# Kernel optimization log

Hardware: AMD Instinct MI355X
Metric: run time of the kernel (lower is better)

Reference implementation:

```python
import jax, jax.numpy as jnp
import numpy as np

IMAGE_SIZE = 800
OUT = 50          # feature map size
FEAT = 512
SCALES = (2.0, 4.0, 6.0)
RATIOS = (0.5, 1.0, 1.5)
A = len(SCALES) * len(RATIOS)          # 9 anchors per cell
POS_THR, NEG_THR = 0.7, 0.3
W_CONF, W_REG = 1.0, 5.0
SCALE = IMAGE_SIZE // OUT              # 16, stride of feature map


def _anchor_base():
    # order: ratio outer loop, scale inner loop (matches get_anchor_base)
    ws = jnp.array([s * r for r in RATIOS for s in SCALES], jnp.float32)  # [A]
    hs = jnp.array([s for r in RATIOS for s in SCALES], jnp.float32)      # [A]
    cx = (jnp.arange(OUT, dtype=jnp.float32) + 0.5)[:, None, None]        # grid dim0 -> x
    cy = (jnp.arange(OUT, dtype=jnp.float32) + 0.5)[None, :, None]        # grid dim1 -> y
    xmin = jnp.clip(cx - ws / 2, 0.0, OUT)
    xmax = jnp.clip(cx + ws / 2, 0.0, OUT)
    ymin = jnp.clip(cy - hs / 2, 0.0, OUT)
    ymax = jnp.clip(cy + hs / 2, 0.0, OUT)
    shp = (OUT, OUT, A)
    base = jnp.stack([jnp.broadcast_to(xmin, shp), jnp.broadcast_to(ymin, shp),
                      jnp.broadcast_to(xmax, shp), jnp.broadcast_to(ymax, shp)], axis=-1)
    return base.reshape(-1, 4)         # [N,4], N = OUT*OUT*A = 22500


def _iou(anchors, gt):
    # anchors [N,4], gt [B,M,4] (xyxy) -> iou [B,N,M]
    a = anchors[None, :, None, :]
    g = gt[:, None, :, :]
    ix1 = jnp.maximum(a[..., 0], g[..., 0]); iy1 = jnp.maximum(a[..., 1], g[..., 1])
    ix2 = jnp.minimum(a[..., 2], g[..., 2]); iy2 = jnp.minimum(a[..., 3], g[..., 3])
    inter = jnp.clip(ix2 - ix1, 0.0) * jnp.clip(iy2 - iy1, 0.0)
    area_a = (a[..., 2] - a[..., 0]) * (a[..., 3] - a[..., 1])
    area_g = (g[..., 2] - g[..., 0]) * (g[..., 3] - g[..., 1])
    return inter / (area_a + area_g - inter + 1e-8)


def _smooth_l1(d):
    ad = jnp.abs(d)
    return jnp.where(ad < 1.0, 0.5 * d * d, ad - 0.5)


def setup_inputs() -> dict:
    key = jax.random.key(0)
    ks = jax.random.split(key, 8)
    B, M = 16, 16
    features = jax.random.normal(ks[0], (B, FEAT, OUT, OUT), jnp.float32)
    # valid GT boxes in image coords: centers in [100,700], sizes in [32,200]
    cxy = jax.random.uniform(ks[1], (B, M, 2), jnp.float32, 100.0, 700.0)
    wh = jax.random.uniform(ks[2], (B, M, 2), jnp.float32, 32.0, 200.0)
    x1y1 = jnp.clip(cxy - wh / 2, 0.0, IMAGE_SIZE)
    x2y2 = jnp.clip(cxy + wh / 2, 0.0, IMAGE_SIZE)
    gt_boxes = jnp.concatenate([x1y1, x2y2], axis=-1)
    w1 = jax.random.normal(ks[3], (FEAT, FEAT, 3, 3), jnp.float32) * 0.02
    b1 = jnp.zeros((FEAT,), jnp.float32)
    w_cls = jax.random.normal(ks[4], (A, FEAT), jnp.float32) * 0.02
    b_cls = jnp.zeros((A,), jnp.float32)
    w_box = jax.random.normal(ks[5], (4 * A, FEAT), jnp.float32) * 0.02
    b_box = jnp.zeros((4 * A,), jnp.float32)
    return {"features": features, "gt_boxes": gt_boxes, "w1": w1, "b1": b1,
            "w_cls": w_cls, "b_cls": b_cls, "w_box": w_box, "b_box": b_box}


def reference(features, gt_boxes, w1, b1, w_cls, b_cls, w_box, b_box):
    B = features.shape[0]
    anchors = _anchor_base()                                   # [N,4]
    N = anchors.shape[0]

    # --- conv tower ---
    x = jax.lax.conv_general_dilated(features, w1, (1, 1), 'SAME') + b1[None, :, None, None]
    cls_map = jnp.einsum('bchw,ac->bahw', x, w_cls) + b_cls[None, :, None, None]   # [B,A,H,W]
    box_map = jnp.einsum('bchw,dc->bdhw', x, w_box) + b_box[None, :, None, None]   # [B,4A,H,W]
    logits = jnp.transpose(cls_map, (0, 2, 3, 1)).reshape(B, N)                    # [B,N]
    pred_off = jnp.transpose(box_map.reshape(B, A, 4, OUT, OUT), (0, 3, 4, 1, 2)).reshape(B, N, 4)

    # --- project gt to feature-map (anchor) coords, 'p2a' ---
    gt = gt_boxes / SCALE                                       # [B,M,4]

    # --- anchor/GT assignment ---
    iou = _iou(anchors, gt)                                     # [B,N,M]
    max_per_gt = jnp.max(iou, axis=1, keepdims=True)            # best anchor per gt
    pos_mask = ((iou == max_per_gt) & (max_per_gt > 0)) | (iou > POS_THR)  # [B,N,M]
    pos_mask = pos_mask.astype(jnp.float32)
    n_pos = jnp.maximum(pos_mask.sum(), 1.0)

    # --- gt offsets (standard tx,ty,tw,th) for every (anchor,gt) pair ---
    acx = (anchors[:, 0] + anchors[:, 2]) / 2
    acy = (anchors[:, 1] + anchors[:, 3]) / 2
    aw = jnp.maximum(anchors[:, 2] - anchors[:, 0], 1e-6)
    ah = jnp.maximum(anchors[:, 3] - anchors[:, 1], 1e-6)
    gcx = (gt[..., 0] + gt[..., 2]) / 2                         # [B,M]
    gcy = (gt[..., 1] + gt[..., 3]) / 2
    gw = jnp.maximum(gt[..., 2] - gt[..., 0], 1e-6)
    gh = jnp.maximum(gt[..., 3] - gt[..., 1], 1e-6)
    tx = (gcx[:, None, :] - acx[None, :, None]) / aw[None, :, None]   # [B,N,M]
    ty = (gcy[:, None, :] - acy[None, :, None]) / ah[None, :, None]
    tw = jnp.log(gw[:, None, :] / aw[None, :, None])
    th = jnp.log(gh[:, None, :] / ah[None, :, None])
    gt_off = jnp.stack([tx, ty, tw, th], axis=-1)               # [B,N,M,4]

    diff = gt_off - pred_off[:, :, None, :]
    reg_loss = (pos_mask[..., None] * _smooth_l1(diff)).sum() / (4.0 * n_pos)

    # --- classification loss: BCE-with-logits; positives=1, negatives=0 ---
    pos_loss = (pos_mask * jax.nn.softplus(-logits)[:, :, None]).sum() / n_pos
    neg_anchor = jnp.all(iou < NEG_THR, axis=2).astype(jnp.float32)   # [B,N]
    n_neg = jnp.maximum(neg_anchor.sum(), 1.0)
    neg_loss = (neg_anchor * jax.nn.softplus(logits)).sum() / n_neg
    cls_loss = 0.5 * (pos_loss + neg_loss)

    total_rpn_loss = W_CONF * cls_loss + W_REG * reg_loss

    # --- proposals from predicted offsets for all anchors ---
    pcx = acx[None, :] + pred_off[..., 0] * aw[None, :]
    pcy = acy[None, :] + pred_off[..., 1] * ah[None, :]
    pw = aw[None, :] * jnp.exp(pred_off[..., 2])
    ph = ah[None, :] * jnp.exp(pred_off[..., 3])
    proposals = jnp.stack([pcx - pw / 2, pcy - ph / 2, pcx + pw / 2, pcy + ph / 2], axis=-1)  # [B,N,4]

    return total_rpn_loss, proposals
```

## Files before the change

kernel.cpp:

```cpp
#include <hip/hip_runtime.h>
#include <hip/hip_bf16.h>
#include <stdint.h>

using bf16x8 = __attribute__((ext_vector_type(8))) __bf16;
using f32x4  = __attribute__((ext_vector_type(4))) float;

#define FT_POS_B 1024
#define W2_CHUNK_B 34560

__device__ __forceinline__ unsigned short f2bf(float f) {
  union { float f; unsigned u; } x; x.f = f;
  unsigned r = x.u + 0x7fffu + ((x.u >> 16) & 1u);
  return (unsigned short)(r >> 16);
}

__device__ __forceinline__ void gl_lds16(const void* g, void* l) {
  __builtin_amdgcn_global_load_lds(
      (const __attribute__((address_space(1))) void*)g,
      (__attribute__((address_space(3))) void*)l, 16, 0, 0);
}

__device__ __forceinline__ float sl1(float d) {
  float ad = fabsf(d);
  return ad < 1.f ? 0.5f * d * d : ad - 0.5f;
}
__device__ __forceinline__ float softplus_f(float x) {
  return fmaxf(x, 0.f) + log1pf(expf(-fabsf(x)));
}

__device__ __forceinline__ void anchor_strict(int n, float& ax1, float& ay1,
                                              float& ax2, float& ay2) {
  int ii = n / 450;
  int rem = n - ii * 450;
  int jj = rem / 9;
  int a  = rem - jj * 9;
  const float SC[3] = {2.f, 4.f, 6.f};
  const float RA[3] = {0.5f, 1.f, 1.5f};
  float w = __fmul_rn(SC[a % 3], RA[a / 3]);
  float h = SC[a % 3];
  float cx = __fadd_rn((float)ii, 0.5f);
  float cy = __fadd_rn((float)jj, 0.5f);
  float wh = __fmul_rn(w, 0.5f), hh = __fmul_rn(h, 0.5f);
  ax1 = fminf(fmaxf(__fsub_rn(cx, wh), 0.f), 50.f);
  ax2 = fminf(fmaxf(__fadd_rn(cx, wh), 0.f), 50.f);
  ay1 = fminf(fmaxf(__fsub_rn(cy, hh), 0.f), 50.f);
  ay2 = fminf(fmaxf(__fadd_rn(cy, hh), 0.f), 50.f);
}
__device__ __forceinline__ float iou_strict(float ax1, float ay1, float ax2, float ay2,
                                            float aarea, const float* __restrict__ g) {
  float gx1 = __fmul_rn(g[0], 0.0625f), gy1 = __fmul_rn(g[1], 0.0625f);
  float gx2 = __fmul_rn(g[2], 0.0625f), gy2 = __fmul_rn(g[3], 0.0625f);
  float ix1 = fmaxf(ax1, gx1), iy1 = fmaxf(ay1, gy1);
  float ix2 = fminf(ax2, gx2), iy2 = fminf(ay2, gy2);
  float inter = __fmul_rn(fmaxf(__fsub_rn(ix2, ix1), 0.f),
                          fmaxf(__fsub_rn(iy2, iy1), 0.f));
  float garea = __fmul_rn(__fsub_rn(gx2, gx1), __fsub_rn(gy2, gy1));
  float denom = __fadd_rn(__fsub_rn(__fadd_rn(aarea, garea), inter), 1e-8f);
  return __fdiv_rn(inter, denom);
}

__global__ __launch_bounds__(256) void k_featT(const float* __restrict__ feat,
                                               char* __restrict__ featT2) {
  const int tile = blockIdx.x;
  const int h    = blockIdx.y;
  const int b    = blockIdx.z;
  const int tid  = threadIdx.x;
  if (tile == 79) {
    uint4 z = {0, 0, 0, 0};
    for (int u = tid; u < 204 * 8; u += 256) {
      int p = u >> 3, rec = u & 7;
      int ip, jp;
      if (p < 52)       { ip = 0;       jp = p; }
      else if (p < 104) { ip = 51;      jp = p - 52; }
      else if (p < 154) { ip = p - 103; jp = 0; }
      else              { ip = p - 153; jp = 51; }
      char* dst = featT2 + (size_t)((b * 52 + ip) * 52 + jp) * FT_POS_B
                + (h * 8 + rec) * 64;
      *(uint4*)(dst)      = z;
      *(uint4*)(dst + 16) = z;
      *(uint4*)(dst + 32) = z;
      *(uint4*)(dst + 48) = z;
    }
    return;
  }
  __shared__ __align__(16) unsigned short sT[32][264];
  const int pos0 = tile * 32;
  const float* fb = feat + (size_t)b * 1280000 + (size_t)h * 256 * 2500;
  const int psub = (tid & 7) * 4;
  const int cio  = tid >> 3;
#pragma unroll
  for (int it = 0; it < 8; ++it) {
    int ci = it * 32 + cio;
    int p = pos0 + psub;
    float4 v;
    if (p + 3 < 2500) {
      v = *(const float4*)(fb + (size_t)ci * 2500 + p);
    } else {
      v.x = fb[(size_t)ci * 2500 + min(p + 0, 2499)];
      v.y = fb[(size_t)ci * 2500 + min(p + 1, 2499)];
      v.z = fb[(size_t)ci * 2500 + min(p + 2, 2499)];
      v.w = fb[(size_t)ci * 2500 + min(p + 3, 2499)];
    }
    sT[psub + 0][ci] = f2bf(v.x);
    sT[psub + 1][ci] = f2bf(v.y);
    sT[psub + 2][ci] = f2bf(v.z);
    sT[psub + 3][ci] = f2bf(v.w);
  }
  __syncthreads();
  {
    int p = tid >> 3, rec = tid & 7;
    int gp = pos0 + p;
    if (gp < 2500) {
      int i = gp / 50, j = gp - i * 50;
      char* dst = featT2 + (size_t)((b * 52 + i + 1) * 52 + (j + 1)) * FT_POS_B
                + (h * 8 + rec) * 64;
      const uint4* src = (const uint4*)&sT[p][rec * 32];
      uint4 a0 = src[0], a1 = src[1], a2 = src[2], a3 = src[3];
      *(uint4*)(dst)      = a0;
      *(uint4*)(dst + 16) = a1;
      *(uint4*)(dst + 32) = a2;
      *(uint4*)(dst + 48) = a3;
    }
  }
}

__global__ __launch_bounds__(128) void k_weff1(const float* __restrict__ w1,
                                               const float* __restrict__ wc,
                                               const float* __restrict__ wb,
                                               float* __restrict__ part) {
  __shared__ float sW[48][64];
  const int t = threadIdx.x;
  const int kmem = blockIdx.x * 128 + t;
  const int cz = blockIdx.y;
#pragma unroll
  for (int q = 0; q < 24; ++q) {
    int idx = t + q * 128;
    int co = idx >> 6, cl = idx & 63;
    int c = cz * 64 + cl;
    float v = 0.f;
    if (co < 9) v = wc[co * 512 + c];
    else if (co < 45) v = wb[(co - 9) * 512 + c];
    sW[co][cl] = v;
  }
  __syncthreads();
  float acc[48];
#pragma unroll
  for (int co = 0; co < 48; ++co) acc[co] = 0.f;
  const float* w1p = w1 + (size_t)(cz * 64) * 4608 + kmem;
  for (int c4 = 0; c4 < 64; c4 += 4) {
    float f0 = w1p[(size_t)(c4 + 0) * 4608];
    float f1 = w1p[(size_t)(c4 + 1) * 4608];
    float f2 = w1p[(size_t)(c4 + 2) * 4608];
    float f3 = w1p[(size_t)(c4 + 3) * 4608];
#pragma unroll
    for (int co = 0; co < 48; ++co) {
      float4 wv = *(const float4*)&sW[co][c4];
      acc[co] += wv.x * f0 + wv.y * f1 + wv.z * f2 + wv.w * f3;
    }
  }
  float* dst = part + (size_t)cz * 221184 + kmem;
#pragma unroll
  for (int co = 0; co < 48; ++co) dst[(size_t)co * 4608] = acc[co];
}

__global__ __launch_bounds__(256) void k_weff2(const float* __restrict__ part,
                                               unsigned short* __restrict__ w2) {
  int idx = blockIdx.x * 256 + threadIdx.x;
  int c = idx / 17280;  int r = idx - c * 17280;
  int tap = r / 1920;   int r2 = r - tap * 1920;
  int co = r2 / 40;     int e = r2 - co * 40;
  float s = 0.f;
  if (e < 32) {
    int ci = c * 32 + e;
    const float* p = part + (size_t)co * 4608 + ci * 9 + tap;
#pragma unroll
    for (int cz = 0; cz < 8; ++cz) s += p[(size_t)cz * 221184];
  }
  w2[idx] = f2bf(s);
}

__global__ __launch_bounds__(64) void k_bias(const float* __restrict__ wc,
                                             const float* __restrict__ wb,
                                             const float* __restrict__ b1,
                                             const float* __restrict__ bc,
                                             const float* __restrict__ bbx,
                                             float* __restrict__ bias_eff) {
  int co = blockIdx.x, l = threadIdx.x;
  float s = 0.f;
#pragma unroll
  for (int q = 0; q < 8; ++q) {
    int c = q * 64 + l;
    float wv = co < 9 ? wc[co * 512 + c] : (co < 45 ? wb[(co - 9) * 512 + c] : 0.f);
    s += wv * b1[c];
  }
  for (int o = 32; o; o >>= 1) s += __shfl_down(s, o, 64);
  if (l == 0)
    bias_eff[co] = s + (co < 9 ? bc[co] : (co < 45 ? bbx[co - 9] : 0.f));
}

__global__ __launch_bounds__(256) void k_iou(const float* __restrict__ gt_boxes,
                                             unsigned* __restrict__ mx) {
  int b = blockIdx.y;
  int n = blockIdx.x * 256 + threadIdx.x;
  float lm[16];
#pragma unroll
  for (int m = 0; m < 16; ++m) lm[m] = 0.f;
  if (n < 22500) {
    float ax1, ay1, ax2, ay2;
    anchor_strict(n, ax1, ay1, ax2, ay2);
    float aarea = __fmul_rn(__fsub_rn(ax2, ax1), __fsub_rn(ay2, ay1));
#pragma unroll
    for (int m = 0; m < 16; ++m)
      lm[m] = iou_strict(ax1, ay1, ax2, ay2, aarea, gt_boxes + (b * 16 + m) * 4);
  }
  __shared__ float red[4][16];
#pragma unroll
  for (int m = 0; m < 16; ++m) {
    float v = lm[m];
    for (int o = 32; o; o >>= 1) v = fmaxf(v, __shfl_down(v, o, 64));
    if ((threadIdx.x & 63) == 0) red[threadIdx.x >> 6][m] = v;
  }
  __syncthreads();
  if (threadIdx.x < 16) {
    float v = fmaxf(fmaxf(red[0][threadIdx.x], red[1][threadIdx.x]),
                    fmaxf(red[2][threadIdx.x], red[3][threadIdx.x]));
    atomicMax(mx + b * 16 + threadIdx.x, __float_as_uint(v));
  }
}

__global__ __launch_bounds__(256) void k_conv(const char* __restrict__ featT2,
                                              const char* __restrict__ w2,
                                              const float* __restrict__ beff,
                                              float* __restrict__ oh) {
  __shared__ __align__(16) char sF[2][19456];
  __shared__ __align__(16) char sA[2][34816];
  const int tid = threadIdx.x, lane = tid & 63, w = tid >> 6;
  const int bx = blockIdx.x;
  const int b = bx >> 4, tl = bx & 15, tr = tl >> 2, tc = tl & 3;
  const int i0 = tr * 13 - (tr == 3 ? 1 : 0);
  const int TI = (tr >= 2) ? 12 : 13;
  const int j0 = tc * 13 - (tc == 3 ? 1 : 0);
  const int TJ = (tc >= 2) ? 12 : 13;
  const int TJ2 = TJ + 2;
  const int mcount = TI * TJ;
  const int pieces = (TI + 2) * TJ2 * 5;

  const char* srcF[5];
#pragma unroll
  for (int k = 0; k < 5; ++k) {
    int s = w * 5 + k;
    int pi = s * 64 + lane;
    if (pi >= pieces) pi = pieces - 1;
    int pos = pi / 5, pc = pi - pos * 5;
    if (pc > 3) pc = 3;
    int hi = pos / TJ2, hj = pos - hi * TJ2;
    srcF[k] = featT2 + (size_t)((b * 52 + i0 + hi) * 52 + (j0 + hj)) * FT_POS_B + pc * 16;
  }
  int idxB[3];
#pragma unroll
  for (int bf = 0; bf < 3; ++bf) {
    int p = (w * 3 + bf) * 16 + (lane & 15);
    if (p >= mcount) p = mcount - 1;
    int di = p / TJ, dj = p - di * TJ;
    idxB[bf] = (di * TJ2 + dj) * 80 + (lane >> 4) * 16;
  }
  const int aoff = (lane & 15) * 80 + (lane >> 4) * 16;
  int toff[9];
#pragma unroll
  for (int tp = 0; tp < 9; ++tp) toff[tp] = ((tp / 3) * TJ2 + (tp % 3)) * 80;

  f32x4 acc[3][3] = {};

  auto stage = [&](int c, int pb) {
#pragma unroll
    for (int k = 0; k < 5; ++k) {
      int s = w * 5 + k;
      if (s < 18) gl_lds16(srcF[k] + (size_t)c * 64, sF[pb] + s * 1024);
    }
#pragma unroll
    for (int k = 0; k < 9; ++k) {
      int s = w + 4 * k;
      if (s < 34)
        gl_lds16(w2 + (size_t)c * W2_CHUNK_B + s * 1024 + lane * 16, sA[pb] + s * 1024);
    }
  };

  stage(0, 0);
  __builtin_amdgcn_s_waitcnt(0);
  __syncthreads();

  for (int c = 0; c < 16; ++c) {
    int pb = c & 1;
    if (c < 15) stage(c + 1, pb ^ 1);
    const char* fA = sA[pb];
    const char* fB = sF[pb];
#pragma unroll
    for (int tp = 0; tp < 9; ++tp) {
      bf16x8 av[3], bv[3];
#pragma unroll
      for (int cf = 0; cf < 3; ++cf)
        av[cf] = *(const bf16x8*)(fA + tp * 3840 + cf * 1280 + aoff);
#pragma unroll
      for (int bf = 0; bf < 3; ++bf)
        bv[bf] = *(const bf16x8*)(fB + idxB[bf] + toff[tp]);
#pragma unroll
      for (int cf = 0; cf < 3; ++cf)
#pragma unroll
        for (int bf = 0; bf < 3; ++bf)
          acc[cf][bf] = __builtin_amdgcn_mfma_f32_16x16x32_bf16(av[cf], bv[bf], acc[cf][bf], 0, 0, 0);
    }
    __builtin_amdgcn_s_waitcnt(0);
    __syncthreads();
  }

  f32x4 bias[3];
#pragma unroll
  for (int cf = 0; cf < 3; ++cf)
    bias[cf] = *(const f32x4*)(beff + cf * 16 + (lane >> 4) * 4);
#pragma unroll
  for (int bf = 0; bf < 3; ++bf) {
    int p = (w * 3 + bf) * 16 + (lane & 15);
    if (p >= mcount) continue;
    int di = p / TJ, dj = p - di * TJ;
    int gm = (b * 50 + i0 + di) * 50 + (j0 + dj);
#pragma unroll
    for (int cf = 0; cf < 3; ++cf) {
      f32x4 v = acc[cf][bf];
#pragma unroll
      for (int r = 0; r < 4; ++r) v[r] += bias[cf][r];
      *(f32x4*)(oh + (size_t)gm * 48 + cf * 16 + (lane >> 4) * 4) = v;
    }
  }
}

__global__ __launch_bounds__(256) void k_loss(const float* __restrict__ gt_boxes,
                                              const unsigned* __restrict__ mxbuf,
                                              const float* __restrict__ oh,
                                              float* __restrict__ accum,
                                              float* __restrict__ dout) {
  int b = blockIdx.y;
  int n = blockIdx.x * 256 + threadIdx.x;
  float s_np = 0.f, s_reg = 0.f, s_pos = 0.f, s_nc = 0.f, s_nl = 0.f;
  if (n < 22500) {
    float ax1, ay1, ax2, ay2;
    anchor_strict(n, ax1, ay1, ax2, ay2);
    float aarea = __fmul_rn(__fsub_rn(ax2, ax1), __fsub_rn(ay2, ay1));
    float acx = (ax1 + ax2) * 0.5f, acy = (ay1 + ay2) * 0.5f;
    float aw = fmaxf(ax2 - ax1, 1e-6f), ah = fmaxf(ay2 - ay1, 1e-6f);
    int ii = n / 450, rem = n - ii * 450, jj = rem / 9, a = rem - jj * 9;
    const float* row = oh + ((size_t)(b * 2500 + ii * 50 + jj)) * 48;
    float logit = row[a];
    float p0 = row[9 + a * 4], p1 = row[10 + a * 4];
    float p2 = row[11 + a * 4], p3 = row[12 + a * 4];
    int npos = 0;
    bool allneg = true;
#pragma unroll
    for (int m = 0; m < 16; ++m) {
      const float* g = gt_boxes + (b * 16 + m) * 4;
      float iou = iou_strict(ax1, ay1, ax2, ay2, aarea, g);
      float mxv = __uint_as_float(mxbuf[b * 16 + m]);
      bool pos = ((iou == mxv) && (mxv > 0.f)) || (iou > 0.7f);
      if (iou >= 0.3f) allneg = false;
      if (pos) {
        ++npos;
        float gx1 = g[0] * 0.0625f, gy1 = g[1] * 0.0625f;
        float gx2 = g[2] * 0.0625f, gy2 = g[3] * 0.0625f;
        float gcx = (gx1 + gx2) * 0.5f, gcy = (gy1 + gy2) * 0.5f;
        float gw = fmaxf(gx2 - gx1, 1e-6f), gh = fmaxf(gy2 - gy1, 1e-6f);
        float tx = (gcx - acx) / aw, ty = (gcy - acy) / ah;
        float twv = logf(gw / aw), thv = logf(gh / ah);
        s_reg += sl1(tx - p0) + sl1(ty - p1) + sl1(twv - p2) + sl1(thv - p3);
      }
    }
    s_np = (float)npos;
    s_pos = (float)npos * softplus_f(-logit);
    if (allneg) { s_nc = 1.f; s_nl = softplus_f(logit); }
    float pcx = acx + p0 * aw, pcy = acy + p1 * ah;
    float pw = aw * expf(p2), ph = ah * expf(p3);
    float* o = dout + 1 + ((size_t)b * 22500 + n) * 4;
    o[0] = pcx - pw * 0.5f;
    o[1] = pcy - ph * 0.5f;
    o[2] = pcx + pw * 0.5f;
    o[3] = pcy + ph * 0.5f;
  }
  float vals[5] = {s_np, s_reg, s_pos, s_nc, s_nl};
  __shared__ float red[4][5];
#pragma unroll
  for (int q = 0; q < 5; ++q) {
    float v = vals[q];
    for (int o = 32; o; o >>= 1) v += __shfl_down(v, o, 64);
    if ((threadIdx.x & 63) == 0) red[threadIdx.x >> 6][q] = v;
  }
  __syncthreads();
  if (threadIdx.x < 5) {
    float v = red[0][threadIdx.x] + red[1][threadIdx.x] +
              red[2][threadIdx.x] + red[3][threadIdx.x];
    atomicAdd(accum + threadIdx.x, v);
  }
}

__global__ void k_fin(const float* __restrict__ accum, float* __restrict__ dout) {
  if (threadIdx.x == 0 && blockIdx.x == 0) {
    float np = fmaxf(accum[0], 1.f);
    float nn = fmaxf(accum[3], 1.f);
    float loss = 0.5f * (accum[2] / np + accum[4] / nn) + 5.f * (accum[1] / (4.f * np));
    dout[0] = loss;
  }
}

extern "C" void kernel_launch(void* const* d_in, const int* in_sizes, int n_in,
                              void* d_out, int out_size, void* d_ws, size_t ws_size,
                              hipStream_t stream) {
  const float* features = (const float*)d_in[0];
  const float* gt_boxes = (const float*)d_in[1];
  const float* w1    = (const float*)d_in[2];
  const float* b1    = (const float*)d_in[3];
  const float* w_cls = (const float*)d_in[4];
  const float* b_cls = (const float*)d_in[5];
  const float* w_box = (const float*)d_in[6];
  const float* b_box = (const float*)d_in[7];
  float* out = (float*)d_out;
  char* ws = (char*)d_ws;

  char*           featT2 = ws;
  unsigned short* w2     = (unsigned short*)(ws + 44302336);
  float*          wpart  = (float*)(ws + 44855296);
  float*          oh     = (float*)(ws + 51933184);
  float*          beff   = (float*)(ws + 59613184);
  unsigned*       mx     = (unsigned*)(ws + 59613376);
  float*          accum  = (float*)(ws + 59614400);

  hipMemsetAsync(ws + 59613376, 0, 1056, stream);

  k_featT<<<dim3(80, 2, 16), 256, 0, stream>>>(features, featT2);
  k_weff1<<<dim3(36, 8), 128, 0, stream>>>(w1, w_cls, w_box, wpart);
  k_weff2<<<1080, 256, 0, stream>>>(wpart, w2);
  k_bias<<<48, 64, 0, stream>>>(w_cls, w_box, b1, b_cls, b_box, beff);
  k_iou<<<dim3(88, 16), 256, 0, stream>>>(gt_boxes, mx);
  k_conv<<<256, 256, 0, stream>>>(featT2, (const char*)w2, beff, oh);
  k_loss<<<dim3(88, 16), 256, 0, stream>>>(gt_boxes, mx, oh, accum, out);
  k_fin<<<1, 64, 0, stream>>>(accum, out);
}
```

Baseline: 276.1 us.

## Retile feature transpose and fold memset and bias kernel into others

The feature transpose now uses 128-position by 128-channel tiles with packed ushort4 LDS writes instead of 32-position by 256-channel tiles, which cuts the block count and widens the shared-memory stores. The separate hipMemsetAsync is replaced by zeroing inside the first k_weff1 block, and the k_bias kernel is merged into extra blocks of k_weff2. Together these remove two launches and the memset from the stream. The risk is that the zeroing now depends on k_weff1 running before k_iou, which stream order guarantees, and the LDS row stride of 132 may cause bank conflicts.

```diff
diff --git a/kernel.cpp b/kernel.cpp
--- a/kernel.cpp
+++ b/kernel.cpp
@@ -62,20 +62,20 @@
 __global__ __launch_bounds__(256) void k_featT(const float* __restrict__ feat,
                                                char* __restrict__ featT2) {
   const int tile = blockIdx.x;
-  const int h    = blockIdx.y;
+  const int g    = blockIdx.y;
   const int b    = blockIdx.z;
   const int tid  = threadIdx.x;
-  if (tile == 79) {
+  if (tile == 20) {
     uint4 z = {0, 0, 0, 0};
-    for (int u = tid; u < 204 * 8; u += 256) {
-      int p = u >> 3, rec = u & 7;
+    for (int u = tid; u < 204 * 4; u += 256) {
+      int p = u >> 2, c4 = u & 3;
       int ip, jp;
       if (p < 52)       { ip = 0;       jp = p; }
       else if (p < 104) { ip = 51;      jp = p - 52; }
       else if (p < 154) { ip = p - 103; jp = 0; }
       else              { ip = p - 153; jp = 51; }
       char* dst = featT2 + (size_t)((b * 52 + ip) * 52 + jp) * FT_POS_B
-                + (h * 8 + rec) * 64;
+                + (g * 4 + c4) * 64;
       *(uint4*)(dst)      = z;
       *(uint4*)(dst + 16) = z;
       *(uint4*)(dst + 32) = z;
@@ -83,53 +83,65 @@
     }
     return;
   }
-  __shared__ __align__(16) unsigned short sT[32][264];
-  const int pos0 = tile * 32;
-  const float* fb = feat + (size_t)b * 1280000 + (size_t)h * 256 * 2500;
-  const int psub = (tid & 7) * 4;
-  const int cio  = tid >> 3;
-#pragma unroll
-  for (int it = 0; it < 8; ++it) {
-    int ci = it * 32 + cio;
-    int p = pos0 + psub;
-    float4 v;
-    if (p + 3 < 2500) {
-      v = *(const float4*)(fb + (size_t)ci * 2500 + p);
-    } else {
-      v.x = fb[(size_t)ci * 2500 + min(p + 0, 2499)];
-      v.y = fb[(size_t)ci * 2500 + min(p + 1, 2499)];
-      v.z = fb[(size_t)ci * 2500 + min(p + 2, 2499)];
-      v.w = fb[(size_t)ci * 2500 + min(p + 3, 2499)];
-    }
-    sT[psub + 0][ci] = f2bf(v.x);
-    sT[psub + 1][ci] = f2bf(v.y);
-    sT[psub + 2][ci] = f2bf(v.z);
-    sT[psub + 3][ci] = f2bf(v.w);
+  __shared__ __align__(16) unsigned short sT[128 * 132];
+  const int pos0 = tile * 128;
+  const float* fb = feat + (size_t)b * 1280000 + (size_t)(g * 128) * 2500;
+  const int pq = tid & 31;
+  const int rg = tid >> 5;
+  const int p  = pos0 + pq * 4;
+#pragma unroll
+  for (int it = 0; it < 4; ++it) {
+    int cb = it * 32 + rg * 4;
+    float vv[4][4];
+#pragma unroll
+    for (int q = 0; q < 4; ++q) {
+      const float* src = fb + (size_t)(cb + q) * 2500 + p;
+      if (p + 3 < 2500) {
+        float4 v = *(const float4*)src;
+        vv[q][0] = v.x; vv[q][1] = v.y; vv[q][2] = v.z; vv[q][3] = v.w;
+      } else {
+#pragma unroll
+        for (int e = 0; e < 4; ++e)
+          vv[q][e] = fb[(size_t)(cb + q) * 2500 + min(p + e, 2499)];
+      }
+    }
+#pragma unroll
+    for (int pp = 0; pp < 4; ++pp) {
+      ushort4 pk;
+      pk.x = f2bf(vv[0][pp]); pk.y = f2bf(vv[1][pp]);
+      pk.z = f2bf(vv[2][pp]); pk.w = f2bf(vv[3][pp]);
+      *(ushort4*)&sT[(pq * 4 + pp) * 132 + cb] = pk;
+    }
   }
   __syncthreads();
-  {
-    int p = tid >> 3, rec = tid & 7;
-    int gp = pos0 + p;
-    if (gp < 2500) {
-      int i = gp / 50, j = gp - i * 50;
-      char* dst = featT2 + (size_t)((b * 52 + i + 1) * 52 + (j + 1)) * FT_POS_B
-                + (h * 8 + rec) * 64;
-      const uint4* src = (const uint4*)&sT[p][rec * 32];
-      uint4 a0 = src[0], a1 = src[1], a2 = src[2], a3 = src[3];
-      *(uint4*)(dst)      = a0;
-      *(uint4*)(dst + 16) = a1;
-      *(uint4*)(dst + 32) = a2;
-      *(uint4*)(dst + 48) = a3;
-    }
+#pragma unroll
+  for (int q2 = 0; q2 < 2; ++q2) {
+    int u = tid + q2 * 256;
+    int pr = u >> 2, ch = u & 3;
+    int gp = pos0 + pr;
+    if (gp >= 2500) continue;
+    int i = gp / 50, j = gp - i * 50;
+    char* dst = featT2 + (size_t)((b * 52 + i + 1) * 52 + (j + 1)) * FT_POS_B
+              + (g * 4 + ch) * 64;
+    const uint4* src = (const uint4*)&sT[pr * 132 + ch * 32];
+    uint4 a0 = src[0], a1 = src[1], a2 = src[2], a3 = src[3];
+    *(uint4*)(dst)      = a0;
+    *(uint4*)(dst + 16) = a1;
+    *(uint4*)(dst + 32) = a2;
+    *(uint4*)(dst + 48) = a3;
   }
 }
 
 __global__ __launch_bounds__(128) void k_weff1(const float* __restrict__ w1,
                                                const float* __restrict__ wc,
                                                const float* __restrict__ wb,
-                                               float* __restrict__ part) {
+                                               float* __restrict__ part,
+                                               unsigned* __restrict__ zbuf) {
+  const int t = threadIdx.x;
+  if (blockIdx.x == 0 && blockIdx.y == 0) {
+    for (int idx = t; idx < 264; idx += 128) zbuf[idx] = 0u;
+  }
   __shared__ float sW[48][64];
-  const int t = threadIdx.x;
   const int kmem = blockIdx.x * 128 + t;
   const int cz = blockIdx.y;
 #pragma unroll
@@ -164,7 +176,29 @@
 }
 
 __global__ __launch_bounds__(256) void k_weff2(const float* __restrict__ part,
-                                               unsigned short* __restrict__ w2) {
+                                               unsigned short* __restrict__ w2,
+                                               const float* __restrict__ wc,
+                                               const float* __restrict__ wb,
+                                               const float* __restrict__ b1,
+                                               const float* __restrict__ bc,
+                                               const float* __restrict__ bbx,
+                                               float* __restrict__ bias_eff) {
+  if (blockIdx.x >= 1080) {
+    int co = blockIdx.x - 1080;
+    int l = threadIdx.x;
+    if (l >= 64) return;
+    float s = 0.f;
+#pragma unroll
+    for (int q = 0; q < 8; ++q) {
+      int c = q * 64 + l;
+      float wv = co < 9 ? wc[co * 512 + c] : (co < 45 ? wb[(co - 9) * 512 + c] : 0.f);
+      s += wv * b1[c];
+    }
+    for (int o = 32; o; o >>= 1) s += __shfl_down(s, o, 64);
+    if (l == 0)
+      bias_eff[co] = s + (co < 9 ? bc[co] : (co < 45 ? bbx[co - 9] : 0.f));
+    return;
+  }
   int idx = blockIdx.x * 256 + threadIdx.x;
   int c = idx / 17280;  int r = idx - c * 17280;
   int tap = r / 1920;   int r2 = r - tap * 1920;
@@ -177,25 +211,6 @@
     for (int cz = 0; cz < 8; ++cz) s += p[(size_t)cz * 221184];
   }
   w2[idx] = f2bf(s);
-}
-
-__global__ __launch_bounds__(64) void k_bias(const float* __restrict__ wc,
-                                             const float* __restrict__ wb,
-                                             const float* __restrict__ b1,
-                                             const float* __restrict__ bc,
-                                             const float* __restrict__ bbx,
-                                             float* __restrict__ bias_eff) {
-  int co = blockIdx.x, l = threadIdx.x;
-  float s = 0.f;
-#pragma unroll
-  for (int q = 0; q < 8; ++q) {
-    int c = q * 64 + l;
-    float wv = co < 9 ? wc[co * 512 + c] : (co < 45 ? wb[(co - 9) * 512 + c] : 0.f);
-    s += wv * b1[c];
-  }
-  for (int o = 32; o; o >>= 1) s += __shfl_down(s, o, 64);
-  if (l == 0)
-    bias_eff[co] = s + (co < 9 ? bc[co] : (co < 45 ? bbx[co - 9] : 0.f));
 }
 
 __global__ __launch_bounds__(256) void k_iou(const float* __restrict__ gt_boxes,
@@ -430,12 +445,9 @@
   unsigned*       mx     = (unsigned*)(ws + 59613376);
   float*          accum  = (float*)(ws + 59614400);
 
-  hipMemsetAsync(ws + 59613376, 0, 1056, stream);
-
-  k_featT<<<dim3(80, 2, 16), 256, 0, stream>>>(features, featT2);
-  k_weff1<<<dim3(36, 8), 128, 0, stream>>>(w1, w_cls, w_box, wpart);
-  k_weff2<<<1080, 256, 0, stream>>>(wpart, w2);
-  k_bias<<<48, 64, 0, stream>>>(w_cls, w_box, b1, b_cls, b_box, beff);
+  k_featT<<<dim3(21, 4, 16), 256, 0, stream>>>(features, featT2);
+  k_weff1<<<dim3(36, 8), 128, 0, stream>>>(w1, w_cls, w_box, wpart, mx);
+  k_weff2<<<1128, 256, 0, stream>>>(wpart, w2, w_cls, w_box, b1, b_cls, b_box, beff);
   k_iou<<<dim3(88, 16), 256, 0, stream>>>(gt_boxes, mx);
   k_conv<<<256, 256, 0, stream>>>(featT2, (const char*)w2, beff, oh);
   k_loss<<<dim3(88, 16), 256, 0, stream>>>(gt_boxes, mx, oh, accum, out);
```

Result: faster. 269.9 us (-2.2%).
